# Kernel tuning notes

Measured on AMD Instinct MI355X. Metric: run time of the kernel, lower is better.

## Reference

```python
import jax, jax.numpy as jnp
import numpy as np

B, S, D = 2, 2048, 1024
H = 16
HD = D // H  # head dim 64


def setup_inputs() -> dict:
    key = jax.random.key(0)
    ks = jax.random.split(key, 7)
    queries = jax.random.normal(ks[0], (B, S, D), dtype=jnp.float32)
    keys = jax.random.normal(ks[1], (B, S, D), dtype=jnp.float32)
    values = jax.random.normal(ks[2], (B, S, D), dtype=jnp.float32)
    scale = 1.0 / np.sqrt(D)
    Wq = jax.random.normal(ks[3], (D, D), dtype=jnp.float32) * scale
    Wk = jax.random.normal(ks[4], (D, D), dtype=jnp.float32) * scale
    Wv = jax.random.normal(ks[5], (D, D), dtype=jnp.float32) * scale
    Wo = jax.random.normal(ks[6], (D, D), dtype=jnp.float32) * scale
    return {"queries": queries, "keys": keys, "values": values,
            "Wq": Wq, "Wk": Wk, "Wv": Wv, "Wo": Wo}


def _split_heads(x):
    # [B,S,D] -> [B,H,S,HD]
    b, s, d = x.shape
    return x.reshape(b, s, H, d // H).transpose(0, 2, 1, 3)


def reference(queries, keys, values, Wq, Wk, Wv, Wo):
    q = _split_heads(queries @ Wq) * (HD ** -0.5)   # [B,H,S,HD]
    k = _split_heads(keys @ Wk)
    v = _split_heads(values @ Wv)
    logits = jnp.einsum('bhqd,bhkd->bhqk', q, k)     # [B,H,S,S]
    weights = jax.nn.softmax(logits, axis=-1)
    ctx = jnp.einsum('bhqk,bhkd->bhqd', weights, v)  # [B,H,S,HD]
    ctx = ctx.transpose(0, 2, 1, 3).reshape(B, S, D)
    return ctx @ Wo
```

## Files before the change

### kernel.cpp

```cpp
#include <hip/hip_runtime.h>
#include <hip/hip_bf16.h>


typedef short s16x8 __attribute__((ext_vector_type(8)));
typedef float f32x4v __attribute__((ext_vector_type(4)));

__device__ inline unsigned short f2bf(float f) {
    union { float f; unsigned int i; } x; x.f = f;
    unsigned int r = x.i + 0x7FFFu + ((x.i >> 16) & 1u);
    return (unsigned short)(r >> 16);
}
__device__ inline unsigned int pkbf(float lo, float hi) {
    return (unsigned int)f2bf(lo) | ((unsigned int)f2bf(hi) << 16);
}

__device__ inline void gld_lds16(const unsigned short* g, unsigned short* l) {
    __builtin_amdgcn_global_load_lds(
        (const __attribute__((address_space(1))) unsigned int*)(const void*)g,
        (__attribute__((address_space(3))) unsigned int*)(void*)l,
        16, 0, 0);
}

__global__ __launch_bounds__(256)
void cvt3(const float* __restrict__ W0, const float* __restrict__ W1, const float* __restrict__ W2,
          unsigned short* __restrict__ T0, unsigned short* __restrict__ T1, unsigned short* __restrict__ T2) {
    const float* W = (blockIdx.z == 0) ? W0 : (blockIdx.z == 1) ? W1 : W2;
    unsigned short* Wt = (blockIdx.z == 0) ? T0 : (blockIdx.z == 1) ? T1 : T2;
    __shared__ __align__(16) unsigned short Ls[64 * 72];
    const int t = threadIdx.x;
    const int k0 = blockIdx.y * 64, n0 = blockIdx.x * 64;
    const int r = t >> 4, c4 = (t & 15) * 4;
    #pragma unroll
    for (int i = 0; i < 4; ++i) {
        float4 wv = *(const float4*)&W[(size_t)(k0 + r + i * 16) * 1024 + n0 + c4];
        Ls[(c4 + 0) * 72 + r + i * 16] = f2bf(wv.x);
        Ls[(c4 + 1) * 72 + r + i * 16] = f2bf(wv.y);
        Ls[(c4 + 2) * 72 + r + i * 16] = f2bf(wv.z);
        Ls[(c4 + 3) * 72 + r + i * 16] = f2bf(wv.w);
    }
    __syncthreads();
    #pragma unroll
    for (int i = 0; i < 2; ++i) {
        const int p = i * 256 + t;
        const int n = p & 63, kc = p >> 6;
        s16x8 v = *(const s16x8*)&Ls[n * 72 + kc * 8];
        const int gn = n0 + n, k = k0 + kc * 8;
        const size_t g = ((size_t)(gn >> 7) * 128 + (k >> 3)) * 128 + (gn & 127);
        *(s16x8*)&Wt[g * 8] = v;
    }
}

__global__ __launch_bounds__(256, 3)
void gemm_qkv(const float* __restrict__ A0, const float* __restrict__ A1, const float* __restrict__ A2,
              const unsigned short* __restrict__ W0, const unsigned short* __restrict__ W1,
              const unsigned short* __restrict__ W2,
              unsigned short* __restrict__ OQ, unsigned short* __restrict__ OK,
              unsigned short* __restrict__ OV, float scaleQ) {
    const int z = blockIdx.z;
    const float* Av = (z == 0) ? A0 : (z == 1) ? A1 : A2;
    const unsigned short* Bsw = (z == 0) ? W0 : (z == 1) ? W1 : W2;
    const float scale = (z == 0) ? scaleQ : 1.0f;

    __shared__ __align__(16) unsigned short Al[1024 * 8];
    __shared__ __align__(16) unsigned short Bl[1024 * 8];
    const int t = threadIdx.x;
    const int lane = t & 63, w = t >> 6;
    const int ln = lane & 15, qd = lane >> 4;
    const int mw = (w & 1) * 64, nw = (w >> 1) * 64;
    const int m0 = blockIdx.y * 128, n0 = blockIdx.x * 128;

    f32x4v acc[4][4] = {};

    for (int k0 = 0; k0 < 1024; k0 += 64) {
        __syncthreads();
        {
            const size_t gb = ((size_t)(n0 >> 7) * 128 + (k0 >> 3)) * 128;
            #pragma unroll
            for (int j = 0; j < 4; ++j)
                gld_lds16(Bsw + (gb + j * 256 + t) * 8, &Bl[(j * 256 + w * 64) * 8]);
        }
        #pragma unroll
        for (int j = 0; j < 4; ++j) {
            const int p = j * 256 + t;
            const int row = p >> 3, kc = p & 7;
            const float* src = Av + (size_t)(m0 + row) * 1024 + k0 + kc * 8;
            float4 f0 = ((const float4*)src)[0];
            float4 f1 = ((const float4*)src)[1];
            uint4 u;
            u.x = pkbf(f0.x, f0.y); u.y = pkbf(f0.z, f0.w);
            u.z = pkbf(f1.x, f1.y); u.w = pkbf(f1.z, f1.w);
            *(uint4*)&Al[(kc * 128 + (row ^ kc)) * 8] = u;
        }
        __syncthreads();

        #pragma unroll
        for (int kk = 0; kk < 2; ++kk) {
            const int kc = kk * 4 + qd;
            s16x8 a[4], b[4];
            #pragma unroll
            for (int mt = 0; mt < 4; ++mt)
                a[mt] = *(const s16x8*)&Al[(kc * 128 + ((mw + mt * 16 + ln) ^ kc)) * 8];
            #pragma unroll
            for (int nt = 0; nt < 4; ++nt)
                b[nt] = *(const s16x8*)&Bl[(kc * 128 + nw + nt * 16 + ln) * 8];
            #pragma unroll
            for (int mt = 0; mt < 4; ++mt)
                #pragma unroll
                for (int nt = 0; nt < 4; ++nt)
                    acc[mt][nt] = __builtin_amdgcn_mfma_f32_16x16x32_bf16(a[mt], b[nt], acc[mt][nt], 0, 0, 0);
        }
    }

    #pragma unroll
    for (int mt = 0; mt < 4; ++mt)
        #pragma unroll
        for (int nt = 0; nt < 4; ++nt)
            #pragma unroll
            for (int i = 0; i < 4; ++i) {
                const int m = m0 + mw + mt * 16 + qd * 4 + i;
                const int n = n0 + nw + nt * 16 + ln;
                const float v = acc[mt][nt][i] * scale;
                const int bh = (m >> 11) * 16 + (n >> 6), s = m & 2047, hd = n & 63;
                if (z == 0) {
                    OQ[((size_t)bh * 2048 + s) * 64 + hd] = f2bf(v);
                } else if (z == 1) {
                    const size_t g = ((size_t)(bh * 32 + (s >> 6)) * 8 + (hd >> 3)) * 64 + (s & 63);
                    OK[g * 8 + (hd & 7)] = f2bf(v);
                } else {
                    const size_t g = ((size_t)(bh * 32 + (s >> 6)) * 8 + ((s >> 3) & 7)) * 64 + hd;
                    OV[g * 8 + (s & 7)] = f2bf(v);
                }
            }
}

__global__ __launch_bounds__(256, 2)
void gemm_out(const unsigned short* __restrict__ Asw, const unsigned short* __restrict__ Bsw,
              float* __restrict__ outF) {
    __shared__ __align__(16) unsigned short Al[1024 * 8];
    __shared__ __align__(16) unsigned short Bl[512 * 8];
    const int t = threadIdx.x;
    const int lane = t & 63, w = t >> 6;
    const int ln = lane & 15, qd = lane >> 4;
    const int mw = (w & 1) * 64, nw = (w >> 1) * 32;
    const int m0 = blockIdx.y * 128, n0 = blockIdx.x * 64;

    f32x4v acc[4][2] = {};

    for (int k0 = 0; k0 < 1024; k0 += 64) {
        __syncthreads();
        {
            const size_t ga = ((size_t)(m0 >> 7) * 128 + (k0 >> 3)) * 128;
            #pragma unroll
            for (int j = 0; j < 4; ++j)
                gld_lds16(Asw + (ga + j * 256 + t) * 8, &Al[(j * 256 + w * 64) * 8]);
        }
        {
            #pragma unroll
            for (int i = 0; i < 2; ++i) {
                const int c = w * 2 + i;
                const size_t gb = ((size_t)(n0 >> 7) * 128 + (k0 >> 3) + c) * 128 + (n0 & 127) + lane;
                gld_lds16(Bsw + gb * 8, &Bl[(c * 64) * 8]);
            }
        }
        __syncthreads();

        #pragma unroll
        for (int kk = 0; kk < 2; ++kk) {
            const int kc = kk * 4 + qd;
            s16x8 a[4], b[2];
            #pragma unroll
            for (int mt = 0; mt < 4; ++mt)
                a[mt] = *(const s16x8*)&Al[(kc * 128 + mw + mt * 16 + ln) * 8];
            #pragma unroll
            for (int nt = 0; nt < 2; ++nt)
                b[nt] = *(const s16x8*)&Bl[(kc * 64 + nw + nt * 16 + ln) * 8];
            #pragma unroll
            for (int mt = 0; mt < 4; ++mt)
                #pragma unroll
                for (int nt = 0; nt < 2; ++nt)
                    acc[mt][nt] = __builtin_amdgcn_mfma_f32_16x16x32_bf16(a[mt], b[nt], acc[mt][nt], 0, 0, 0);
        }
    }

    #pragma unroll
    for (int mt = 0; mt < 4; ++mt)
        #pragma unroll
        for (int nt = 0; nt < 2; ++nt)
            #pragma unroll
            for (int i = 0; i < 4; ++i) {
                const int m = m0 + mw + mt * 16 + qd * 4 + i;
                const int n = n0 + nw + nt * 16 + ln;
                outF[(size_t)m * 1024 + n] = acc[mt][nt][i];
            }
}

__global__ __launch_bounds__(512, 4)
void fattn(const unsigned short* __restrict__ Q, const unsigned short* __restrict__ Ksw,
           const unsigned short* __restrict__ Vsw, unsigned short* __restrict__ ctx) {
    __shared__ __align__(16) unsigned short Ks2[2][512 * 8];
    __shared__ __align__(16) unsigned short Vs2[2][512 * 8];
    __shared__ __align__(16) unsigned short Pw[8][16 * 72];

    const int t = threadIdx.x, lane = t & 63, w = t >> 6;
    const int ln = lane & 15, qd = lane >> 4;
    const int bh = blockIdx.y, m0 = blockIdx.x * 128;
    const size_t head = (size_t)bh * 2048 * 64;

    s16x8 qf[2];
    #pragma unroll
    for (int kk = 0; kk < 2; ++kk)
        qf[kk] = *(const s16x8*)(Q + head + (size_t)(m0 + w * 16 + ln) * 64 + kk * 32 + qd * 8);

    f32x4v accO[4] = {};
    float lsum[4] = {};
    unsigned short* pw = Pw[w];

    {
        const size_t tb = (size_t)bh * 32 * 512;
        gld_lds16(Ksw + (tb + w * 64 + lane) * 8, &Ks2[0][(w * 64) * 8]);
        gld_lds16(Vsw + (tb + w * 64 + lane) * 8, &Vs2[0][(w * 64) * 8]);
    }

    for (int kt = 0; kt < 32; ++kt) {
        const int cur = kt & 1;
        __syncthreads();
        if (kt + 1 < 32) {
            const size_t tb = ((size_t)bh * 32 + kt + 1) * 512;
            gld_lds16(Ksw + (tb + w * 64 + lane) * 8, &Ks2[cur ^ 1][(w * 64) * 8]);
            gld_lds16(Vsw + (tb + w * 64 + lane) * 8, &Vs2[cur ^ 1][(w * 64) * 8]);
        }

        f32x4v accS[4] = {};
        #pragma unroll
        for (int kk = 0; kk < 2; ++kk)
            #pragma unroll
            for (int nt = 0; nt < 4; ++nt) {
                s16x8 b = *(const s16x8*)&Ks2[cur][((kk * 4 + qd) * 64 + nt * 16 + ln) * 8];
                accS[nt] = __builtin_amdgcn_mfma_f32_16x16x32_bf16(qf[kk], b, accS[nt], 0, 0, 0);
            }

        #pragma unroll
        for (int nt = 0; nt < 4; ++nt)
            #pragma unroll
            for (int i = 0; i < 4; ++i) {
                float p = exp2f(accS[nt][i]);
                lsum[i] += p;
                pw[(qd * 4 + i) * 72 + nt * 16 + ln] = f2bf(p);
            }

        #pragma unroll
        for (int kk = 0; kk < 2; ++kk) {
            s16x8 a = *(const s16x8*)&pw[ln * 72 + kk * 32 + qd * 8];
            #pragma unroll
            for (int nt = 0; nt < 4; ++nt) {
                s16x8 b = *(const s16x8*)&Vs2[cur][((kk * 4 + qd) * 64 + nt * 16 + ln) * 8];
                accO[nt] = __builtin_amdgcn_mfma_f32_16x16x32_bf16(a, b, accO[nt], 0, 0, 0);
            }
        }
    }

    #pragma unroll
    for (int i = 0; i < 4; ++i) {
        float s = lsum[i];
        #pragma unroll
        for (int off = 1; off < 16; off <<= 1) s += __shfl_xor(s, off, 64);
        lsum[i] = 1.f / s;
    }

    #pragma unroll
    for (int i = 0; i < 4; ++i) {
        const int mrow = (bh >> 4) * 2048 + m0 + w * 16 + qd * 4 + i;
        #pragma unroll
        for (int nt = 0; nt < 4; ++nt) {
            const int k = (bh & 15) * 64 + nt * 16 + ln;
            const size_t g = ((size_t)(mrow >> 7) * 128 + (k >> 3)) * 128 + (mrow & 127);
            ctx[g * 8 + (k & 7)] = f2bf(accO[nt][i] * lsum[i]);
        }
    }
}

extern "C" void kernel_launch(void* const* d_in, const int* in_sizes, int n_in,
                              void* d_out, int out_size, void* d_ws, size_t ws_size,
                              hipStream_t stream) {
    char* ws = (char*)d_ws;
    unsigned short* Qb  = (unsigned short*)(ws);
    unsigned short* Ksw = (unsigned short*)(ws + ((size_t)8 << 20));
    unsigned short* Vsw = (unsigned short*)(ws + ((size_t)16 << 20));
    unsigned short* Wqt = (unsigned short*)(ws + ((size_t)24 << 20));
    unsigned short* Wkt = (unsigned short*)(ws + ((size_t)26 << 20));
    unsigned short* Wvt = (unsigned short*)(ws + ((size_t)28 << 20));
    unsigned short* ctx = (unsigned short*)(ws + ((size_t)24 << 20));
    unsigned short* Wot = (unsigned short*)(ws);

    cvt3<<<dim3(16, 16, 3), 256, 0, stream>>>((const float*)d_in[3], (const float*)d_in[4],
                                              (const float*)d_in[5], Wqt, Wkt, Wvt);

    gemm_qkv<<<dim3(8, 32, 3), 256, 0, stream>>>(
        (const float*)d_in[0], (const float*)d_in[1], (const float*)d_in[2],
        Wqt, Wkt, Wvt, Qb, Ksw, Vsw, 0.125f * 1.44269504f);

    fattn<<<dim3(16, 32), dim3(512), 0, stream>>>(Qb, Ksw, Vsw, ctx);

    cvt3<<<dim3(16, 16, 1), 256, 0, stream>>>((const float*)d_in[6], nullptr, nullptr,
                                              Wot, nullptr, nullptr);

    gemm_out<<<dim3(16, 32), 256, 0, stream>>>(ctx, Wot, (float*)d_out);
}
```

Measured before the change: 246.0 us.

## Rewrite attention core with 32x32 MFMA and register-resident P via permlane swap

The flash-attention kernel moves from 16x16x32 to 32x32x16 bf16 MFMA, with each wave handling 32 query rows and 4 waves per block instead of 8. It computes S transposed (K as A operand) so the probabilities can be packed with v_cvt_pk_bf16_f32 and rearranged with v_permlane32_swap directly into the A-operand layout for the PV product. This removes the per-wave LDS round trip for P. The trade-off is more registers per thread, fewer waves per block, and a shuffle to gather the row normalisers in the epilogue.

```diff
diff --git a/kernel.cpp b/kernel.cpp
--- a/kernel.cpp
+++ b/kernel.cpp
@@ -4,6 +4,8 @@
 
 typedef short s16x8 __attribute__((ext_vector_type(8)));
 typedef float f32x4v __attribute__((ext_vector_type(4)));
+typedef float f32x16v __attribute__((ext_vector_type(16)));
+typedef unsigned int u32x4v __attribute__((ext_vector_type(4)));
 
 __device__ inline unsigned short f2bf(float f) {
     union { float f; unsigned int i; } x; x.f = f;
@@ -194,31 +196,32 @@
             }
 }
 
-__global__ __launch_bounds__(512, 4)
+__global__ __launch_bounds__(256, 2)
 void fattn(const unsigned short* __restrict__ Q, const unsigned short* __restrict__ Ksw,
            const unsigned short* __restrict__ Vsw, unsigned short* __restrict__ ctx) {
     __shared__ __align__(16) unsigned short Ks2[2][512 * 8];
     __shared__ __align__(16) unsigned short Vs2[2][512 * 8];
-    __shared__ __align__(16) unsigned short Pw[8][16 * 72];
 
     const int t = threadIdx.x, lane = t & 63, w = t >> 6;
-    const int ln = lane & 15, qd = lane >> 4;
+    const int l31 = lane & 31, H = lane >> 5;
     const int bh = blockIdx.y, m0 = blockIdx.x * 128;
     const size_t head = (size_t)bh * 2048 * 64;
 
-    s16x8 qf[2];
-    #pragma unroll
-    for (int kk = 0; kk < 2; ++kk)
-        qf[kk] = *(const s16x8*)(Q + head + (size_t)(m0 + w * 16 + ln) * 64 + kk * 32 + qd * 8);
-
-    f32x4v accO[4] = {};
-    float lsum[4] = {};
-    unsigned short* pw = Pw[w];
+    s16x8 qf[4];
+    #pragma unroll
+    for (int kk = 0; kk < 4; ++kk)
+        qf[kk] = *(const s16x8*)(Q + head + (size_t)(m0 + w * 32 + l31) * 64 + kk * 16 + H * 8);
+
+    f32x16v accO[2] = {};
+    float lsum = 0.f;
 
     {
         const size_t tb = (size_t)bh * 32 * 512;
-        gld_lds16(Ksw + (tb + w * 64 + lane) * 8, &Ks2[0][(w * 64) * 8]);
-        gld_lds16(Vsw + (tb + w * 64 + lane) * 8, &Vs2[0][(w * 64) * 8]);
+        #pragma unroll
+        for (int j = 0; j < 2; ++j) {
+            gld_lds16(Ksw + (tb + j * 256 + t) * 8, &Ks2[0][(j * 256 + w * 64) * 8]);
+            gld_lds16(Vsw + (tb + j * 256 + t) * 8, &Vs2[0][(j * 256 + w * 64) * 8]);
+        }
     }
 
     for (int kt = 0; kt < 32; ++kt) {
@@ -226,55 +229,70 @@
         __syncthreads();
         if (kt + 1 < 32) {
             const size_t tb = ((size_t)bh * 32 + kt + 1) * 512;
-            gld_lds16(Ksw + (tb + w * 64 + lane) * 8, &Ks2[cur ^ 1][(w * 64) * 8]);
-            gld_lds16(Vsw + (tb + w * 64 + lane) * 8, &Vs2[cur ^ 1][(w * 64) * 8]);
-        }
-
-        f32x4v accS[4] = {};
-        #pragma unroll
-        for (int kk = 0; kk < 2; ++kk)
-            #pragma unroll
-            for (int nt = 0; nt < 4; ++nt) {
-                s16x8 b = *(const s16x8*)&Ks2[cur][((kk * 4 + qd) * 64 + nt * 16 + ln) * 8];
-                accS[nt] = __builtin_amdgcn_mfma_f32_16x16x32_bf16(qf[kk], b, accS[nt], 0, 0, 0);
-            }
-
-        #pragma unroll
-        for (int nt = 0; nt < 4; ++nt)
-            #pragma unroll
-            for (int i = 0; i < 4; ++i) {
-                float p = exp2f(accS[nt][i]);
-                lsum[i] += p;
-                pw[(qd * 4 + i) * 72 + nt * 16 + ln] = f2bf(p);
-            }
-
-        #pragma unroll
-        for (int kk = 0; kk < 2; ++kk) {
-            s16x8 a = *(const s16x8*)&pw[ln * 72 + kk * 32 + qd * 8];
-            #pragma unroll
-            for (int nt = 0; nt < 4; ++nt) {
-                s16x8 b = *(const s16x8*)&Vs2[cur][((kk * 4 + qd) * 64 + nt * 16 + ln) * 8];
-                accO[nt] = __builtin_amdgcn_mfma_f32_16x16x32_bf16(a, b, accO[nt], 0, 0, 0);
-            }
-        }
-    }
-
-    #pragma unroll
-    for (int i = 0; i < 4; ++i) {
-        float s = lsum[i];
-        #pragma unroll
-        for (int off = 1; off < 16; off <<= 1) s += __shfl_xor(s, off, 64);
-        lsum[i] = 1.f / s;
-    }
-
-    #pragma unroll
-    for (int i = 0; i < 4; ++i) {
-        const int mrow = (bh >> 4) * 2048 + m0 + w * 16 + qd * 4 + i;
-        #pragma unroll
-        for (int nt = 0; nt < 4; ++nt) {
-            const int k = (bh & 15) * 64 + nt * 16 + ln;
+            #pragma unroll
+            for (int j = 0; j < 2; ++j) {
+                gld_lds16(Ksw + (tb + j * 256 + t) * 8, &Ks2[cur ^ 1][(j * 256 + w * 64) * 8]);
+                gld_lds16(Vsw + (tb + j * 256 + t) * 8, &Vs2[cur ^ 1][(j * 256 + w * 64) * 8]);
+            }
+        }
+
+        f32x16v accS[2] = {};
+        #pragma unroll
+        for (int kk = 0; kk < 4; ++kk)
+            #pragma unroll
+            for (int mt = 0; mt < 2; ++mt) {
+                s16x8 kf = *(const s16x8*)&Ks2[cur][((kk * 2 + H) * 64 + mt * 32 + l31) * 8];
+                accS[mt] = __builtin_amdgcn_mfma_f32_32x32x16_bf16(kf, qf[kk], accS[mt], 0, 0, 0);
+            }
+
+        u32x4v af[4];
+        #pragma unroll
+        for (int mt = 0; mt < 2; ++mt) {
+            float p[16];
+            #pragma unroll
+            for (int r = 0; r < 16; ++r) {
+                p[r] = exp2f(accS[mt][r]);
+                lsum += p[r];
+            }
+            unsigned int C[8];
+            #pragma unroll
+            for (int j = 0; j < 8; ++j)
+                asm("v_cvt_pk_bf16_f32 %0, %1, %2" : "=v"(C[j]) : "v"(p[2 * j]), "v"(p[2 * j + 1]));
+            #pragma unroll
+            for (int pp = 0; pp < 2; ++pp) {
+                unsigned int x0 = C[4 * pp + 0], y0 = C[4 * pp + 2];
+                unsigned int x1 = C[4 * pp + 1], y1 = C[4 * pp + 3];
+                asm("v_permlane32_swap_b32 %0, %1" : "+v"(x0), "+v"(y0));
+                asm("v_permlane32_swap_b32 %0, %1" : "+v"(x1), "+v"(y1));
+                u32x4v a; a.x = x0; a.y = x1; a.z = y0; a.w = y1;
+                af[mt * 2 + pp] = a;
+            }
+        }
+
+        #pragma unroll
+        for (int kk2 = 0; kk2 < 4; ++kk2) {
+            s16x8 a = __builtin_bit_cast(s16x8, af[kk2]);
+            #pragma unroll
+            for (int nt = 0; nt < 2; ++nt) {
+                s16x8 b = *(const s16x8*)&Vs2[cur][((kk2 * 2 + H) * 64 + nt * 32 + l31) * 8];
+                accO[nt] = __builtin_amdgcn_mfma_f32_32x32x16_bf16(a, b, accO[nt], 0, 0, 0);
+            }
+        }
+    }
+
+    lsum += __shfl_xor(lsum, 32, 64);
+    const float inv = 1.f / lsum;
+
+    #pragma unroll
+    for (int r = 0; r < 16; ++r) {
+        const int qloc = (r & 3) + 8 * (r >> 2) + 4 * H;
+        const float rinv = __shfl(inv, qloc, 64);
+        const int mrow = (bh >> 4) * 2048 + m0 + w * 32 + qloc;
+        #pragma unroll
+        for (int nt = 0; nt < 2; ++nt) {
+            const int k = (bh & 15) * 64 + nt * 32 + l31;
             const size_t g = ((size_t)(mrow >> 7) * 128 + (k >> 3)) * 128 + (mrow & 127);
-            ctx[g * 8 + (k & 7)] = f2bf(accO[nt][i] * lsum[i]);
+            ctx[g * 8 + (k & 7)] = f2bf(accO[nt][r] * rinv);
         }
     }
 }
@@ -299,7 +317,7 @@
         (const float*)d_in[0], (const float*)d_in[1], (const float*)d_in[2],
         Wqt, Wkt, Wvt, Qb, Ksw, Vsw, 0.125f * 1.44269504f);
 
-    fattn<<<dim3(16, 32), dim3(512), 0, stream>>>(Qb, Ksw, Vsw, ctx);
+    fattn<<<dim3(16, 32), dim3(256), 0, stream>>>(Qb, Ksw, Vsw, ctx);
 
     cvt3<<<dim3(16, 16, 1), 256, 0, stream>>>((const float*)d_in[6], nullptr, nullptr,
                                               Wot, nullptr, nullptr);
```

After: 241.5 us. About the same (-1.8%).
